# Kernel tuning notes

Measured on AMD Instinct MI355X. Metric: run time of the kernel, lower is better.

## Reference

```python
import jax, jax.numpy as jnp
import numpy as np

B, H, W, C = 16, 32, 32, 256
N = H * W


def setup_inputs() -> dict:
    key = jax.random.key(0)
    ks = jax.random.split(key, 8)
    x = jax.random.normal(ks[0], (B, H, W, C), dtype=jnp.float32)
    # nn.LazyLinear(C): weight (C, C), bias (C,)
    scale = 1.0 / np.sqrt(C)
    Wq = jax.random.uniform(ks[1], (C, C), jnp.float32, -scale, scale)
    bq = jax.random.uniform(ks[2], (C,), jnp.float32, -scale, scale)
    Wk = jax.random.uniform(ks[3], (C, C), jnp.float32, -scale, scale)
    bk = jax.random.uniform(ks[4], (C,), jnp.float32, -scale, scale)
    Wv = jax.random.uniform(ks[5], (C, C), jnp.float32, -scale, scale)
    bv = jax.random.uniform(ks[6], (C,), jnp.float32, -scale, scale)
    # torch.randn(H, H*W, W)
    Wp = jax.random.normal(ks[7], (H, N, W), dtype=jnp.float32)
    return {"x": x, "Wq": Wq, "bq": bq, "Wk": Wk, "bk": bk,
            "Wv": Wv, "bv": bv, "Wp": Wp}


def reference(x, Wq, bq, Wk, bk, Wv, bv, Wp):
    b, h, w, c = x.shape
    n = h * w
    # Linear projections (torch Linear: x @ W^T + b), flatten spatial dims to N tokens
    q = (jnp.einsum('bhwc,dc->bhwd', x, Wq) + bq).reshape(b, n, c)
    k = (jnp.einsum('bhwc,dc->bhwd', x, Wk) + bk).reshape(b, n, c)
    v = (jnp.einsum('bhwc,dc->bhwd', x, Wv) + bv).reshape(b, n, c)
    # Unscaled attention over the N spatial tokens (no 1/sqrt(C) in the original)
    scores = jnp.einsum('bnc,bmc->bnm', q, k)          # (B, N, N)
    attn = jax.nn.softmax(scores, axis=-1)
    qkv = jnp.einsum('bnm,bmc->bnc', attn, v)           # (B, N, C)
    # z = (qkv^T [B,1,C,N] @ Wp [H,N,W]).transpose(-2,-1) -> (B, H, W, C)
    z = jnp.einsum('bnc,hnw->bhwc', qkv, Wp)
    return z
```

## Files before the change

kernel.cpp:

```cpp
#include <hip/hip_runtime.h>
#include <hip/hip_bf16.h>

#define BB 16
#define NN 1024
#define CC 256

typedef __attribute__((ext_vector_type(8))) short bf16x8;
typedef __attribute__((ext_vector_type(4))) short s16x4;
typedef __attribute__((ext_vector_type(4))) float f32x4;

#define GPTR(p) ((const __attribute__((address_space(1))) void*)(p))
#define LPTR(p) ((__attribute__((address_space(3))) void*)(p))

__device__ __forceinline__ unsigned short f2bf(float f) {
  union { float f; unsigned u; } v; v.f = f;
  unsigned r = v.u + 0x7FFFu + ((v.u >> 16) & 1u);
  return (unsigned short)(r >> 16);
}

__device__ __forceinline__ bf16x8 pack8(f32x4 a, f32x4 b) {
  bf16x8 o;
  o[0] = (short)f2bf(a[0]); o[1] = (short)f2bf(a[1]);
  o[2] = (short)f2bf(a[2]); o[3] = (short)f2bf(a[3]);
  o[4] = (short)f2bf(b[0]); o[5] = (short)f2bf(b[1]);
  o[6] = (short)f2bf(b[2]); o[7] = (short)f2bf(b[3]);
  return o;
}

template <int BIAS_MODE, int F32OUT>
__global__ __launch_bounds__(256) void gemm_tile(
    const unsigned short* __restrict__ A, int lda, long sA,
    const unsigned short* __restrict__ Bt, int ldb, long sB,
    const float* __restrict__ bias,
    void* __restrict__ Out, int ldo, long sO, int K) {
  __shared__ unsigned short As[2][2 * 128 * 32];
  __shared__ unsigned short Bs[2][2 * 64 * 32];
  int b = blockIdx.x;
  int m0 = blockIdx.y * 128;
  int n0 = blockIdx.z * 64;
  int t = threadIdx.x;
  int w = t >> 6, lane = t & 63;
  int wm = (w >> 1) * 64, wn = (w & 1) * 32;
  int r = lane & 15, g = lane >> 4;

  const unsigned short* Ab = A + (long)b * sA;
  const unsigned short* Bb = Bt + (long)b * sB;

  int srow = t >> 2;
  int scolsw = (((t & 3) ^ ((t >> 2) & 3))) * 8;
  int ag = ((g ^ (r & 3))) * 8;

  f32x4 acc[4][2];
#pragma unroll
  for (int i = 0; i < 4; i++)
#pragma unroll
    for (int j = 0; j < 2; j++) acc[i][j] = (f32x4){0.f, 0.f, 0.f, 0.f};

#define STAGE_GT(buf, k0)                                                     \
  do {                                                                        \
    _Pragma("unroll") for (int kh = 0; kh < 2; kh++) {                        \
      _Pragma("unroll") for (int jj = 0; jj < 2; jj++) {                      \
        __builtin_amdgcn_global_load_lds(                                     \
            GPTR(Ab + (long)(m0 + srow + jj * 64) * lda + (k0) + kh * 32 +    \
                 scolsw),                                                     \
            LPTR(&As[buf][kh * 4096 + jj * 2048 + t * 8]), 16, 0, 0);         \
      }                                                                       \
      __builtin_amdgcn_global_load_lds(                                       \
          GPTR(Bb + (long)(n0 + srow) * ldb + (k0) + kh * 32 + scolsw),       \
          LPTR(&Bs[buf][kh * 2048 + t * 8]), 16, 0, 0);                       \
    }                                                                         \
  } while (0)

  int nt = K >> 6;
  STAGE_GT(0, 0);
  for (int tt = 0; tt < nt; ++tt) {
    int cb = tt & 1;
    if (tt < nt - 1) {
      STAGE_GT(cb ^ 1, (tt + 1) * 64);
      asm volatile("s_waitcnt vmcnt(6)" ::: "memory");
    } else {
      asm volatile("s_waitcnt vmcnt(0)" ::: "memory");
    }
    __builtin_amdgcn_sched_barrier(0);
    __builtin_amdgcn_s_barrier();
    __builtin_amdgcn_sched_barrier(0);
#pragma unroll
    for (int kh = 0; kh < 2; kh++) {
      bf16x8 af[4], bfr[2];
#pragma unroll
      for (int ti = 0; ti < 4; ti++)
        af[ti] = *(const bf16x8*)&As[cb][kh * 4096 + (wm + ti * 16 + r) * 32 + ag];
#pragma unroll
      for (int tj = 0; tj < 2; tj++)
        bfr[tj] = *(const bf16x8*)&Bs[cb][kh * 2048 + (wn + tj * 16 + r) * 32 + ag];
#pragma unroll
      for (int ti = 0; ti < 4; ti++)
#pragma unroll
        for (int tj = 0; tj < 2; tj++)
          acc[ti][tj] = __builtin_amdgcn_mfma_f32_16x16x32_bf16(af[ti], bfr[tj], acc[ti][tj], 0, 0, 0);
    }
    __builtin_amdgcn_s_barrier();
  }
#undef STAGE_GT

#pragma unroll
  for (int ti = 0; ti < 4; ti++) {
#pragma unroll
    for (int tj = 0; tj < 2; tj++) {
      int col = n0 + wn + tj * 16 + r;
      float bc = (BIAS_MODE == 1) ? bias[col] : 0.0f;
#pragma unroll
      for (int rr = 0; rr < 4; rr++) {
        int row = m0 + wm + ti * 16 + g * 4 + rr;
        float val = acc[ti][tj][rr] + bc;
        long oidx = (long)b * sO + (long)row * ldo + col;
        if (F32OUT)
          ((float*)Out)[oidx] = val;
        else
          ((unsigned short*)Out)[oidx] = f2bf(val);
      }
    }
  }
}

__global__ __launch_bounds__(256) void gemm_qkv(
    const float* __restrict__ x,
    const float* __restrict__ Wq, const float* __restrict__ Wk,
    const float* __restrict__ Wv,
    const float* __restrict__ bq, const float* __restrict__ bk,
    const float* __restrict__ bv,
    const float* __restrict__ Wp,
    unsigned short* __restrict__ Qb, unsigned short* __restrict__ Kb,
    unsigned short* __restrict__ Vtb, unsigned short* __restrict__ Amat) {
  __shared__ unsigned short As[2 * 128 * 32];
  __shared__ unsigned short Bs[2 * 128 * 32];

  if (blockIdx.z == 6) {
    float* tile = (float*)As;
    int id = blockIdx.x * 8 + blockIdx.y;
#pragma unroll 1
    for (int u = 0; u < 8; u++) {
      int wb = id * 8 + u;
      int h = wb >> 5;
      int n0w = (wb & 31) * 32;
#pragma unroll
      for (int j = 0; j < 4; j++) {
        int idx = threadIdx.x + j * 256;
        int a = idx >> 5, wc = idx & 31;
        tile[a * 33 + wc] = Wp[(size_t)h * (NN * 32) + (size_t)(n0w + a) * 32 + wc];
      }
      __syncthreads();
#pragma unroll
      for (int j = 0; j < 4; j++) {
        int idx = threadIdx.x + j * 256;
        int wc = idx >> 5, a = idx & 31;
        Amat[(size_t)(h * 32 + wc) * NN + n0w + a] = f2bf(tile[a * 33 + wc]);
      }
      __syncthreads();
    }
    return;
  }

  int b = blockIdx.x;
  int m0 = blockIdx.y * 128;
  int n0 = blockIdx.z * 128;
  int t = threadIdx.x;
  int w = t >> 6, lane = t & 63;
  int wm = (w >> 1) * 64, wn = (w & 1) * 64;
  int r = lane & 15, g = lane >> 4;

  const float* Ab = x + (long)b * NN * CC;
  int srow = t >> 2;
  int scol = (t & 3) * 8;
  int sb = srow * 32 + (((t & 3) ^ (srow & 3)) * 8);
  int ag = ((g ^ (r & 3))) * 8;

  const float* Wsel[2];
  int wrow[2];
#pragma unroll
  for (int jj = 0; jj < 2; jj++) {
    int nbase = n0 + jj * 64;
    int seg = nbase >> 8;
    Wsel[jj] = (seg == 0) ? Wq : (seg == 1 ? Wk : Wv);
    wrow[jj] = (nbase + srow) & 255;
  }

  f32x4 acc[4][4];
#pragma unroll
  for (int i = 0; i < 4; i++)
#pragma unroll
    for (int j = 0; j < 4; j++) acc[i][j] = (f32x4){0.f, 0.f, 0.f, 0.f};

  f32x4 pa[4][2], pw[4][2];
#pragma unroll
  for (int kh = 0; kh < 2; kh++)
#pragma unroll
    for (int jj = 0; jj < 2; jj++) {
      const float* asrc = Ab + (long)(m0 + srow + jj * 64) * CC + kh * 32 + scol;
      pa[kh * 2 + jj][0] = *(const f32x4*)asrc;
      pa[kh * 2 + jj][1] = *(const f32x4*)(asrc + 4);
      const float* wsrc = Wsel[jj] + (long)wrow[jj] * CC + kh * 32 + scol;
      pw[kh * 2 + jj][0] = *(const f32x4*)wsrc;
      pw[kh * 2 + jj][1] = *(const f32x4*)(wsrc + 4);
    }

  for (int k0 = 0; k0 < CC; k0 += 64) {
    if (k0) __builtin_amdgcn_s_barrier();
#pragma unroll
    for (int kh = 0; kh < 2; kh++)
#pragma unroll
      for (int jj = 0; jj < 2; jj++) {
        *(bf16x8*)&As[kh * 4096 + jj * 2048 + sb] =
            pack8(pa[kh * 2 + jj][0], pa[kh * 2 + jj][1]);
        *(bf16x8*)&Bs[kh * 4096 + jj * 2048 + sb] =
            pack8(pw[kh * 2 + jj][0], pw[kh * 2 + jj][1]);
      }
    if (k0 < CC - 64) {
#pragma unroll
      for (int kh = 0; kh < 2; kh++)
#pragma unroll
        for (int jj = 0; jj < 2; jj++) {
          const float* asrc =
              Ab + (long)(m0 + srow + jj * 64) * CC + k0 + 64 + kh * 32 + scol;
          pa[kh * 2 + jj][0] = *(const f32x4*)asrc;
          pa[kh * 2 + jj][1] = *(const f32x4*)(asrc + 4);
          const float* wsrc =
              Wsel[jj] + (long)wrow[jj] * CC + k0 + 64 + kh * 32 + scol;
          pw[kh * 2 + jj][0] = *(const f32x4*)wsrc;
          pw[kh * 2 + jj][1] = *(const f32x4*)(wsrc + 4);
        }
    }
    asm volatile("s_waitcnt lgkmcnt(0)" ::: "memory");
    __builtin_amdgcn_sched_barrier(0);
    __builtin_amdgcn_s_barrier();
    __builtin_amdgcn_sched_barrier(0);
#pragma unroll
    for (int kh = 0; kh < 2; kh++) {
      bf16x8 af[4], bfr[4];
#pragma unroll
      for (int ti = 0; ti < 4; ti++)
        af[ti] = *(const bf16x8*)&As[kh * 4096 + (wm + ti * 16 + r) * 32 + ag];
#pragma unroll
      for (int tj = 0; tj < 4; tj++)
        bfr[tj] = *(const bf16x8*)&Bs[kh * 4096 + (wn + tj * 16 + r) * 32 + ag];
#pragma unroll
      for (int ti = 0; ti < 4; ti++)
#pragma unroll
        for (int tj = 0; tj < 4; tj++)
          acc[ti][tj] = __builtin_amdgcn_mfma_f32_16x16x32_bf16(af[ti], bfr[tj], acc[ti][tj], 0, 0, 0);
    }
  }

  int sege = (n0 + wn) >> 8;
  const float* bsel = (sege == 0) ? bq : (sege == 1 ? bk : bv);
  int seg = n0 >> 8;
#pragma unroll
  for (int ti = 0; ti < 4; ti++) {
#pragma unroll
    for (int tj = 0; tj < 4; tj++) {
      int col = n0 + wn + tj * 16 + r;
      int c = col & 255;
      float bc = bsel[c];
#pragma unroll
      for (int rr = 0; rr < 4; rr++) {
        int row = m0 + wm + ti * 16 + g * 4 + rr;
        float val = acc[ti][tj][rr] + bc;
        long base = (long)b * NN * CC;
        if (seg == 0) {
          Qb[base + (long)row * CC + c] = f2bf(val);
        } else if (seg == 1) {
          Kb[base + ((long)(c >> 5) * NN + row) * 32 + (c & 31)] = f2bf(val);
        } else {
          Vtb[base + ((((long)(c >> 4) * 128 + (row >> 3)) * 16 + (c & 15)) * 8 + (row & 7))] = f2bf(val);
        }
      }
    }
  }
}

__global__ __launch_bounds__(512, 2) void attn_fused(
    const unsigned short* __restrict__ Q,
    const unsigned short* __restrict__ Kt,
    const unsigned short* __restrict__ Vt,
    unsigned short* __restrict__ QKVt) {
  __shared__ unsigned short ShBuf[64 * 1024];
  __shared__ float red[8][64];
  int b = blockIdx.x;
  int n0 = blockIdx.y * 64;
  int t = threadIdx.x;
  int w = t >> 6, lane = t & 63;
  int r = lane & 15, g = lane >> 4;

  const unsigned short* kslab = Kt + (long)b * NN * CC + w * 128 * 32;
  unsigned short* wbuf0 = &ShBuf[w * 4096];
  unsigned short* wbuf1 = &ShBuf[32768 + w * 4096];

  const unsigned short* qbase = Q + ((long)b * NN + n0 + r) * CC + g * 8;

#pragma unroll
  for (int j = 0; j < 8; j++)
    __builtin_amdgcn_global_load_lds(GPTR(kslab + j * 512 + lane * 8),
                                     LPTR(wbuf0 + j * 512 + lane * 8), 16, 0, 0);
  bf16x8 qa[4];
#pragma unroll
  for (int rt = 0; rt < 4; rt++)
    qa[rt] = *(const bf16x8*)(qbase + rt * 16 * CC);

  f32x4 acc[4][8];
#pragma unroll
  for (int i = 0; i < 4; i++)
#pragma unroll
    for (int j = 0; j < 8; j++) acc[i][j] = (f32x4){0.f, 0.f, 0.f, 0.f};

#pragma unroll
  for (int kk = 0; kk < 8; kk++) {
    unsigned short* cur = (kk & 1) ? wbuf1 : wbuf0;
    unsigned short* nxt = (kk & 1) ? wbuf0 : wbuf1;
    if (kk < 7) {
      const unsigned short* src = kslab + (long)(kk + 1) * (NN * 32);
#pragma unroll
      for (int j = 0; j < 8; j++)
        __builtin_amdgcn_global_load_lds(GPTR(src + j * 512 + lane * 8),
                                         LPTR(nxt + j * 512 + lane * 8), 16, 0, 0);
      asm volatile("s_waitcnt vmcnt(8)" ::: "memory");
    } else {
      asm volatile("s_waitcnt vmcnt(0)" ::: "memory");
    }
    __builtin_amdgcn_sched_barrier(0);
    bf16x8 qn[4];
    if (kk < 7) {
#pragma unroll
      for (int rt = 0; rt < 4; rt++)
        qn[rt] = *(const bf16x8*)(qbase + (kk + 1) * 32 + rt * 16 * CC);
    }
    __builtin_amdgcn_s_setprio(1);
#pragma unroll
    for (int ct = 0; ct < 8; ct++) {
      bf16x8 kf = *(const bf16x8*)&cur[(ct * 16 + r) * 32 + g * 8];
#pragma unroll
      for (int rt = 0; rt < 4; rt++)
        acc[rt][ct] = __builtin_amdgcn_mfma_f32_16x16x32_bf16(qa[rt], kf, acc[rt][ct], 0, 0, 0);
    }
    __builtin_amdgcn_s_setprio(0);
    if (kk < 7) {
#pragma unroll
      for (int rt = 0; rt < 4; rt++) qa[rt] = qn[rt];
    }
    __builtin_amdgcn_sched_barrier(0);
  }

  const unsigned short* vbase = Vt + (long)b * NN * CC;
  int cw = w * 32;
  bf16x8 brp[2];
#pragma unroll
  for (int bt = 0; bt < 2; bt++) {
    long vidx = (((long)((cw >> 4) + bt) * 128 + g) * 16 + r) * 8;
    brp[bt] = *(const bf16x8*)(vbase + vidx);
  }
  __builtin_amdgcn_sched_barrier(0);

  float mrow[4][4];
#pragma unroll
  for (int rt = 0; rt < 4; rt++) {
#pragma unroll
    for (int rr = 0; rr < 4; rr++) {
      float m = acc[rt][0][rr];
#pragma unroll
      for (int ct = 1; ct < 8; ct++) m = fmaxf(m, acc[rt][ct][rr]);
#pragma unroll
      for (int d = 1; d < 16; d <<= 1) m = fmaxf(m, __shfl_xor(m, d, 64));
      mrow[rt][rr] = m;
    }
  }
  if (r == 0) {
#pragma unroll
    for (int rt = 0; rt < 4; rt++)
#pragma unroll
      for (int rr = 0; rr < 4; rr++)
        red[w][rt * 16 + g * 4 + rr] = mrow[rt][rr];
  }
  __syncthreads();
#pragma unroll
  for (int rt = 0; rt < 4; rt++) {
#pragma unroll
    for (int rr = 0; rr < 4; rr++) {
      int row = rt * 16 + g * 4 + rr;
      float m = red[0][row];
#pragma unroll
      for (int w2 = 1; w2 < 8; w2++) m = fmaxf(m, red[w2][row]);
      mrow[rt][rr] = m;
    }
  }
  __syncthreads();
  float ssum[4][4];
#pragma unroll
  for (int rt = 0; rt < 4; rt++) {
#pragma unroll
    for (int rr = 0; rr < 4; rr++) {
      float s = 0.f;
#pragma unroll
      for (int ct = 0; ct < 8; ct++) {
        float e = exp2f((acc[rt][ct][rr] - mrow[rt][rr]) * 1.44269504088896f);
        acc[rt][ct][rr] = e;
        s += e;
      }
#pragma unroll
      for (int d = 1; d < 16; d <<= 1) s += __shfl_xor(s, d, 64);
      ssum[rt][rr] = s;
    }
  }
  if (r == 0) {
#pragma unroll
    for (int rt = 0; rt < 4; rt++)
#pragma unroll
      for (int rr = 0; rr < 4; rr++)
        red[w][rt * 16 + g * 4 + rr] = ssum[rt][rr];
  }
  __syncthreads();
#pragma unroll
  for (int rt = 0; rt < 4; rt++) {
#pragma unroll
    for (int rr = 0; rr < 4; rr++) {
      int prow = rt * 16 + g * 4 + rr;
      float s = 0.f;
#pragma unroll
      for (int w2 = 0; w2 < 8; w2++) s += red[w2][prow];
      float inv = 1.0f / s;
      int sw = prow & 7;
#pragma unroll
      for (int ct = 0; ct < 8; ct++) {
        int col = w * 128 + ct * 16 + r;
        int chunk = (col >> 3) ^ sw;
        ShBuf[prow * 1024 + chunk * 8 + (col & 7)] = f2bf(acc[rt][ct][rr] * inv);
      }
    }
  }
  __syncthreads();

  f32x4 o[4][2];
#pragma unroll
  for (int i = 0; i < 4; i++)
#pragma unroll
    for (int j = 0; j < 2; j++) o[i][j] = (f32x4){0.f, 0.f, 0.f, 0.f};

#pragma unroll 4
  for (int m0 = 0; m0 < NN; m0 += 32) {
    bf16x8 ar[4], br[2];
    br[0] = brp[0]; br[1] = brp[1];
    if (m0 + 32 < NN) {
#pragma unroll
      for (int bt = 0; bt < 2; bt++) {
        long vidx = (((long)((cw >> 4) + bt) * 128 + ((m0 + 32) >> 3) + g) * 16 + r) * 8;
        brp[bt] = *(const bf16x8*)(vbase + vidx);
      }
    }
#pragma unroll
    for (int rt = 0; rt < 4; rt++) {
      int prow = rt * 16 + r;
      int chunk = ((m0 >> 3) + g) ^ (prow & 7);
      ar[rt] = *(const bf16x8*)&ShBuf[prow * 1024 + chunk * 8];
    }
    __builtin_amdgcn_s_setprio(1);
#pragma unroll
    for (int rt = 0; rt < 4; rt++)
#pragma unroll
      for (int bt = 0; bt < 2; bt++)
        o[rt][bt] = __builtin_amdgcn_mfma_f32_16x16x32_bf16(ar[rt], br[bt], o[rt][bt], 0, 0, 0);
    __builtin_amdgcn_s_setprio(0);
  }

  unsigned short* obase = QKVt + (long)b * NN * CC;
#pragma unroll
  for (int rt = 0; rt < 4; rt++) {
#pragma unroll
    for (int bt = 0; bt < 2; bt++) {
      int c = cw + bt * 16 + r;
      int n = n0 + rt * 16 + g * 4;
      s16x4 pk;
      pk.x = (short)f2bf(o[rt][bt][0]);
      pk.y = (short)f2bf(o[rt][bt][1]);
      pk.z = (short)f2bf(o[rt][bt][2]);
      pk.w = (short)f2bf(o[rt][bt][3]);
      *(s16x4*)(obase + (long)c * NN + n) = pk;
    }
  }
}

extern "C" void kernel_launch(void* const* d_in, const int* in_sizes, int n_in,
                              void* d_out, int out_size, void* d_ws, size_t ws_size,
                              hipStream_t stream) {
  const float* x  = (const float*)d_in[0];
  const float* Wq = (const float*)d_in[1];
  const float* bq = (const float*)d_in[2];
  const float* Wk = (const float*)d_in[3];
  const float* bk = (const float*)d_in[4];
  const float* Wv = (const float*)d_in[5];
  const float* bv = (const float*)d_in[6];
  const float* Wp = (const float*)d_in[7];
  float* out = (float*)d_out;

  const long BNC = (long)BB * NN * CC;

  char* p = (char*)d_ws;
  unsigned short* Amat  = (unsigned short*)p; p += (long)NN * NN * 2;
  unsigned short* Qb    = (unsigned short*)p; p += BNC * 2;
  unsigned short* Ktb   = (unsigned short*)p; p += BNC * 2;
  unsigned short* Vtb   = (unsigned short*)p; p += BNC * 2;
  unsigned short* QKVt  = (unsigned short*)p; p += BNC * 2;

  gemm_qkv<<<dim3(BB, 8, 7), 256, 0, stream>>>(
      x, Wq, Wk, Wv, bq, bk, bv, Wp, Qb, Ktb, Vtb, Amat);

  attn_fused<<<dim3(BB, NN / 64), 512, 0, stream>>>(Qb, Ktb, Vtb, QKVt);

  gemm_tile<0, 1><<<dim3(BB, 8, 4), 256, 0, stream>>>(
      Amat, NN, 0L, QKVt, NN, (long)NN * CC, nullptr,
      out, CC, (long)NN * CC, NN);
}
```

Before: 150.4 us.

## Pre-cast QKV GEMM inputs to bf16 and stage via direct global-to-LDS loads

Adds a separate preprocessing kernel that converts x, Wq/Wk/Wv to bf16 and gathers the biases into one contiguous buffer. The QKV GEMM then streams bf16 tiles straight into LDS with global_load_lds in a double-buffered pipeline (K-step 32), replacing the register-staged fp32 loads and in-kernel packing, and raises MFMA wave priority. This removes conversion work and register pressure from the GEMM but adds an extra launch plus a full read/write pass over x (about 8 MB read, 8 MB write).

```diff
diff --git a/kernel.cpp b/kernel.cpp
--- a/kernel.cpp
+++ b/kernel.cpp
@@ -18,13 +18,31 @@
   return (unsigned short)(r >> 16);
 }
 
-__device__ __forceinline__ bf16x8 pack8(f32x4 a, f32x4 b) {
-  bf16x8 o;
-  o[0] = (short)f2bf(a[0]); o[1] = (short)f2bf(a[1]);
-  o[2] = (short)f2bf(a[2]); o[3] = (short)f2bf(a[3]);
-  o[4] = (short)f2bf(b[0]); o[5] = (short)f2bf(b[1]);
-  o[6] = (short)f2bf(b[2]); o[7] = (short)f2bf(b[3]);
-  return o;
+#define NCAST 17155
+__global__ __launch_bounds__(256) void preprocess(
+    const float* __restrict__ x,
+    const float* __restrict__ Wq, const float* __restrict__ Wk,
+    const float* __restrict__ Wv,
+    const float* __restrict__ bq, const float* __restrict__ bk,
+    const float* __restrict__ bv,
+    unsigned short* __restrict__ xb,
+    unsigned short* __restrict__ wqkvb,
+    float* __restrict__ bqkv) {
+  const int NX = BB * NN * CC;
+  const int NW = CC * CC;
+  int i = blockIdx.x * 256 + threadIdx.x;
+  if (i < NX) { xb[i] = f2bf(x[i]); return; }
+  int j = i - NX;
+  if (j < 3 * NW) {
+    const float* w = (j < NW) ? Wq : (j < 2 * NW ? Wk : Wv);
+    wqkvb[j] = f2bf(w[j % NW]);
+    return;
+  }
+  int jj = j - 3 * NW;
+  if (jj < 3 * CC) {
+    const float* bb = (jj < CC) ? bq : (jj < 2 * CC ? bk : bv);
+    bqkv[jj] = bb[jj % CC];
+  }
 }
 
 template <int BIAS_MODE, int F32OUT>
@@ -124,16 +142,14 @@
 }
 
 __global__ __launch_bounds__(256) void gemm_qkv(
-    const float* __restrict__ x,
-    const float* __restrict__ Wq, const float* __restrict__ Wk,
-    const float* __restrict__ Wv,
-    const float* __restrict__ bq, const float* __restrict__ bk,
-    const float* __restrict__ bv,
+    const unsigned short* __restrict__ A,
+    const unsigned short* __restrict__ Bt,
+    const float* __restrict__ bias,
     const float* __restrict__ Wp,
     unsigned short* __restrict__ Qb, unsigned short* __restrict__ Kb,
     unsigned short* __restrict__ Vtb, unsigned short* __restrict__ Amat) {
-  __shared__ unsigned short As[2 * 128 * 32];
-  __shared__ unsigned short Bs[2 * 128 * 32];
+  __shared__ unsigned short As[2][128 * 32];
+  __shared__ unsigned short Bs[2][128 * 32];
 
   if (blockIdx.z == 6) {
     float* tile = (float*)As;
@@ -169,98 +185,71 @@
   int wm = (w >> 1) * 64, wn = (w & 1) * 64;
   int r = lane & 15, g = lane >> 4;
 
-  const float* Ab = x + (long)b * NN * CC;
-  int srow = t >> 2;
-  int scol = (t & 3) * 8;
-  int sb = srow * 32 + (((t & 3) ^ (srow & 3)) * 8);
+  const unsigned short* Ab = A + (long)b * NN * CC;
+  int seg = n0 >> 8;
+  const unsigned short* Bb = Bt + (long)(seg << 8) * CC;
+  int nrow0 = n0 & 255;
+
   int ag = ((g ^ (r & 3))) * 8;
 
-  const float* Wsel[2];
-  int wrow[2];
-#pragma unroll
-  for (int jj = 0; jj < 2; jj++) {
-    int nbase = n0 + jj * 64;
-    int seg = nbase >> 8;
-    Wsel[jj] = (seg == 0) ? Wq : (seg == 1 ? Wk : Wv);
-    wrow[jj] = (nbase + srow) & 255;
-  }
-
   f32x4 acc[4][4];
 #pragma unroll
   for (int i = 0; i < 4; i++)
 #pragma unroll
     for (int j = 0; j < 4; j++) acc[i][j] = (f32x4){0.f, 0.f, 0.f, 0.f};
 
-  f32x4 pa[4][2], pw[4][2];
-#pragma unroll
-  for (int kh = 0; kh < 2; kh++)
-#pragma unroll
-    for (int jj = 0; jj < 2; jj++) {
-      const float* asrc = Ab + (long)(m0 + srow + jj * 64) * CC + kh * 32 + scol;
-      pa[kh * 2 + jj][0] = *(const f32x4*)asrc;
-      pa[kh * 2 + jj][1] = *(const f32x4*)(asrc + 4);
-      const float* wsrc = Wsel[jj] + (long)wrow[jj] * CC + kh * 32 + scol;
-      pw[kh * 2 + jj][0] = *(const f32x4*)wsrc;
-      pw[kh * 2 + jj][1] = *(const f32x4*)(wsrc + 4);
-    }
-
-  for (int k0 = 0; k0 < CC; k0 += 64) {
-    if (k0) __builtin_amdgcn_s_barrier();
-#pragma unroll
-    for (int kh = 0; kh < 2; kh++)
-#pragma unroll
-      for (int jj = 0; jj < 2; jj++) {
-        *(bf16x8*)&As[kh * 4096 + jj * 2048 + sb] =
-            pack8(pa[kh * 2 + jj][0], pa[kh * 2 + jj][1]);
-        *(bf16x8*)&Bs[kh * 4096 + jj * 2048 + sb] =
-            pack8(pw[kh * 2 + jj][0], pw[kh * 2 + jj][1]);
-      }
-    if (k0 < CC - 64) {
-#pragma unroll
-      for (int kh = 0; kh < 2; kh++)
-#pragma unroll
-        for (int jj = 0; jj < 2; jj++) {
-          const float* asrc =
-              Ab + (long)(m0 + srow + jj * 64) * CC + k0 + 64 + kh * 32 + scol;
-          pa[kh * 2 + jj][0] = *(const f32x4*)asrc;
-          pa[kh * 2 + jj][1] = *(const f32x4*)(asrc + 4);
-          const float* wsrc =
-              Wsel[jj] + (long)wrow[jj] * CC + k0 + 64 + kh * 32 + scol;
-          pw[kh * 2 + jj][0] = *(const f32x4*)wsrc;
-          pw[kh * 2 + jj][1] = *(const f32x4*)(wsrc + 4);
-        }
-    }
-    asm volatile("s_waitcnt lgkmcnt(0)" ::: "memory");
+#define STAGE_QKV(buf, k0)                                                    \
+  do {                                                                        \
+    _Pragma("unroll") for (int j = 0; j < 2; j++) {                           \
+      int s = (w * 2 + j) * 64 + lane;                                        \
+      int row = s >> 2;                                                       \
+      int csrc = (s & 3) ^ (row & 3);                                         \
+      __builtin_amdgcn_global_load_lds(                                       \
+          GPTR(Ab + (long)(m0 + row) * CC + (k0) + csrc * 8),                 \
+          LPTR(&As[buf][s * 8]), 16, 0, 0);                                   \
+      __builtin_amdgcn_global_load_lds(                                       \
+          GPTR(Bb + (long)(nrow0 + row) * CC + (k0) + csrc * 8),              \
+          LPTR(&Bs[buf][s * 8]), 16, 0, 0);                                   \
+    }                                                                         \
+  } while (0)
+
+  STAGE_QKV(0, 0);
+  for (int tt = 0; tt < 8; ++tt) {
+    int cb = tt & 1;
+    if (tt < 7) {
+      STAGE_QKV(cb ^ 1, (tt + 1) * 32);
+      asm volatile("s_waitcnt vmcnt(4)" ::: "memory");
+    } else {
+      asm volatile("s_waitcnt vmcnt(0)" ::: "memory");
+    }
     __builtin_amdgcn_sched_barrier(0);
     __builtin_amdgcn_s_barrier();
     __builtin_amdgcn_sched_barrier(0);
-#pragma unroll
-    for (int kh = 0; kh < 2; kh++) {
-      bf16x8 af[4], bfr[4];
-#pragma unroll
-      for (int ti = 0; ti < 4; ti++)
-        af[ti] = *(const bf16x8*)&As[kh * 4096 + (wm + ti * 16 + r) * 32 + ag];
+    bf16x8 af[4], bfr[4];
+#pragma unroll
+    for (int ti = 0; ti < 4; ti++)
+      af[ti] = *(const bf16x8*)&As[cb][(wm + ti * 16 + r) * 32 + ag];
+#pragma unroll
+    for (int tj = 0; tj < 4; tj++)
+      bfr[tj] = *(const bf16x8*)&Bs[cb][(wn + tj * 16 + r) * 32 + ag];
+    __builtin_amdgcn_s_setprio(1);
+#pragma unroll
+    for (int ti = 0; ti < 4; ti++)
 #pragma unroll
       for (int tj = 0; tj < 4; tj++)
-        bfr[tj] = *(const bf16x8*)&Bs[kh * 4096 + (wn + tj * 16 + r) * 32 + ag];
-#pragma unroll
-      for (int ti = 0; ti < 4; ti++)
-#pragma unroll
-        for (int tj = 0; tj < 4; tj++)
-          acc[ti][tj] = __builtin_amdgcn_mfma_f32_16x16x32_bf16(af[ti], bfr[tj], acc[ti][tj], 0, 0, 0);
-    }
-  }
-
-  int sege = (n0 + wn) >> 8;
-  const float* bsel = (sege == 0) ? bq : (sege == 1 ? bk : bv);
-  int seg = n0 >> 8;
+        acc[ti][tj] = __builtin_amdgcn_mfma_f32_16x16x32_bf16(af[ti], bfr[tj], acc[ti][tj], 0, 0, 0);
+    __builtin_amdgcn_s_setprio(0);
+    __builtin_amdgcn_s_barrier();
+  }
+#undef STAGE_QKV
+
 #pragma unroll
   for (int ti = 0; ti < 4; ti++) {
 #pragma unroll
     for (int tj = 0; tj < 4; tj++) {
       int col = n0 + wn + tj * 16 + r;
       int c = col & 255;
-      float bc = bsel[c];
+      float bc = bias[col];
 #pragma unroll
       for (int rr = 0; rr < 4; rr++) {
         int row = m0 + wm + ti * 16 + g * 4 + rr;
@@ -502,14 +491,20 @@
   const long BNC = (long)BB * NN * CC;
 
   char* p = (char*)d_ws;
+  unsigned short* xb    = (unsigned short*)p; p += BNC * 2;
+  unsigned short* wqkvb = (unsigned short*)p; p += 3L * CC * CC * 2;
+  float*          bqkv  = (float*)p;          p += 4096;
   unsigned short* Amat  = (unsigned short*)p; p += (long)NN * NN * 2;
   unsigned short* Qb    = (unsigned short*)p; p += BNC * 2;
   unsigned short* Ktb   = (unsigned short*)p; p += BNC * 2;
   unsigned short* Vtb   = (unsigned short*)p; p += BNC * 2;
   unsigned short* QKVt  = (unsigned short*)p; p += BNC * 2;
 
+  preprocess<<<NCAST, 256, 0, stream>>>(x, Wq, Wk, Wv, bq, bk, bv,
+                                        xb, wqkvb, bqkv);
+
   gemm_qkv<<<dim3(BB, 8, 7), 256, 0, stream>>>(
-      x, Wq, Wk, Wv, bq, bk, bv, Wp, Qb, Ktb, Vtb, Amat);
+      xb, wqkvb, bqkv, Wp, Qb, Ktb, Vtb, Amat);
 
   attn_fused<<<dim3(BB, NN / 64), 512, 0, stream>>>(Qb, Ktb, Vtb, QKVt);
 
```

Result: no change. 153.1 us (+1.8%).
